# Performance work log

Hardware: AMD Instinct MI355X
Metric: run time of the kernel (lower is better)

## Reference

```python
import jax, jax.numpy as jnp
import numpy as np

HEADS = 4
DIM_HEAD = 32
SCALE = 10.0
EPS = 1e-12

def l2norm_axis1(t):
    # Faithful to source: default axis=1 -> normalize over the SEQUENCE axis of [B,N,h,d]
    denom = jnp.clip(jnp.linalg.norm(t, ord=2, axis=1, keepdims=True), EPS)
    return t / denom

def setup_inputs() -> dict:
    key = jax.random.key(0)
    k1, k2, k3 = jax.random.split(key, 3)
    B, N, C = 4, 4096, 128
    dim = HEADS * DIM_HEAD  # 128
    x = jax.random.normal(k1, (B, N, C), dtype=jnp.float32)
    W_qkv = jax.random.normal(k2, (C, 3 * dim), dtype=jnp.float32) * (1.0 / np.sqrt(C))
    W_out = jax.random.normal(k3, (dim, C), dtype=jnp.float32) * (1.0 / np.sqrt(dim))
    b_out = jnp.zeros((C,), dtype=jnp.float32)
    return {"x": x, "W_qkv": W_qkv, "W_out": W_out, "b_out": b_out}

def reference(x, W_qkv, W_out, b_out):
    B, N, C = x.shape
    # 1x1 conv == per-token linear
    qkv = jnp.einsum('bnc,ce->bne', x, W_qkv)  # [B,N,3*dim]
    q, k, v = jnp.split(qkv, 3, axis=-1)
    # [B,N,h,d]
    q = q.reshape(B, N, HEADS, DIM_HEAD)
    k = k.reshape(B, N, HEADS, DIM_HEAD)
    v = v.reshape(B, N, HEADS, DIM_HEAD)
    q = l2norm_axis1(q)
    k = l2norm_axis1(k)
    sim = jnp.einsum('bihd,bjhd->bhij', q, k) * SCALE  # [B,h,N,N]
    attn = jax.nn.softmax(sim, axis=-1)
    out = jnp.einsum('bhij,bjhd->bhid', attn, v)  # [B,h,N,d]
    out = out.transpose(0, 2, 1, 3).reshape(B, N, HEADS * DIM_HEAD)  # [B,N,dim]
    return jnp.einsum('bne,ec->bnc', out, W_out) + b_out
```

## Files before the change

### kernel.cpp

```cpp
#include <hip/hip_runtime.h>

typedef short s16x8 __attribute__((ext_vector_type(8)));
typedef short s16x4 __attribute__((ext_vector_type(4)));
typedef float f32x4 __attribute__((ext_vector_type(4)));
typedef float f4 __attribute__((ext_vector_type(4)));
typedef unsigned short u16x4 __attribute__((ext_vector_type(4)));

#define CEXP 14.426950408889634074f

__device__ __forceinline__ unsigned short f2bf(float f) {
    union { float f; unsigned int i; } v; v.f = f;
    unsigned int x = v.i;
    return (unsigned short)((x + 0x7fffu + ((x >> 16) & 1u)) >> 16);
}
__device__ __forceinline__ float bf2f(unsigned short u) {
    union { unsigned int i; float f; } v; v.i = ((unsigned int)u) << 16; return v.f;
}

__device__ __forceinline__ s16x4 pk_bf16x4(float p0, float p1, float p2, float p3) {
#if __has_builtin(__builtin_amdgcn_cvt_pk_bf16_f32)
    typedef __bf16 bf16x2 __attribute__((ext_vector_type(2)));
    union { struct { bf16x2 a, b; } h; s16x4 s; } r;
    r.h.a = __builtin_amdgcn_cvt_pk_bf16_f32(p0, p1);
    r.h.b = __builtin_amdgcn_cvt_pk_bf16_f32(p2, p3);
    return r.s;
#else
    unsigned u0 = __float_as_uint(p0) + 0x8000u;
    unsigned u1 = __float_as_uint(p1) + 0x8000u;
    unsigned u2 = __float_as_uint(p2) + 0x8000u;
    unsigned u3 = __float_as_uint(p3) + 0x8000u;
    union { uint2 u; s16x4 s; } pb;
    pb.u.x = __builtin_amdgcn_perm(u1, u0, 0x07060302u);
    pb.u.y = __builtin_amdgcn_perm(u3, u2, 0x07060302u);
    return pb.s;
#endif
}

__device__ __forceinline__ u16x4 pk4(f4 v) {
    u16x4 r = { f2bf(v[0]), f2bf(v[1]), f2bf(v[2]), f2bf(v[3]) };
    return r;
}

__device__ __forceinline__ void gl_lds16(const void* g, void* l) {
    __builtin_amdgcn_global_load_lds(
        (const __attribute__((address_space(1))) void*)g,
        (__attribute__((address_space(3))) void*)l,
        16, 0, 0);
}

__global__ __launch_bounds__(256) void k_prep(
    const float* __restrict__ Wqkv, const float* __restrict__ Wout,
    unsigned short* __restrict__ Wt, unsigned short* __restrict__ WoT,
    float* __restrict__ sumsqp)
{
    __shared__ float tile[64][65];
    const int blk = blockIdx.x, tid = threadIdx.x;
    if (blk >= 16) {
        sumsqp[(blk - 16) * 256 + tid] = 0.f;
        return;
    }
    const float* src;
    unsigned short* dst;
    int lds_src, k0, n0;
    if (blk < 12) {
        src = Wqkv; dst = Wt; lds_src = 384;
        k0 = (blk & 1) * 64; n0 = (blk >> 1) * 64;
    } else {
        int b = blk - 12;
        src = Wout; dst = WoT; lds_src = 128;
        k0 = (b & 1) * 64; n0 = (b >> 1) * 64;
    }
    const int c = tid & 63, r0 = tid >> 6;
#pragma unroll
    for (int i = 0; i < 16; ++i) {
        int row = i * 4 + r0;
        tile[row][c] = src[(size_t)(k0 + row) * lds_src + n0 + c];
    }
    __syncthreads();
#pragma unroll
    for (int i = 0; i < 16; ++i) {
        int n = i * 4 + r0;
        dst[(size_t)(n0 + n) * 128 + k0 + c] = f2bf(tile[c][n]);
    }
}

__global__ __launch_bounds__(256, 2) void k_qkv(
    const float* __restrict__ x, const unsigned short* __restrict__ Wt,
    unsigned short* __restrict__ Qb, unsigned short* __restrict__ Kb,
    unsigned short* __restrict__ Vt, float* __restrict__ sumsqp)
{
    __shared__ float red[4][64];
    const int tid = threadIdx.x;
    const int wl = tid >> 6, lane = tid & 63;
    const int qd = lane >> 4, nn = lane & 15;
    const int yb = blockIdx.y;
    const int tw0 = blockIdx.x * 64 + wl * 16;

    const float* apf = x + (size_t)(tw0 + nn) * 128 + qd * 8;
    s16x8 af[4];
#pragma unroll
    for (int ks = 0; ks < 4; ++ks) {
        f4 a0 = *(const f4*)(apf + ks * 32);
        f4 a1 = *(const f4*)(apf + ks * 32 + 4);
        union { struct { s16x4 lo, hi; } h; s16x8 v; } u;
        u.h.lo = pk_bf16x4(a0[0], a0[1], a0[2], a0[3]);
        u.h.hi = pk_bf16x4(a1[0], a1[1], a1[2], a1[3]);
        af[ks] = u.v;
    }

    const int b = tw0 >> 12;
    const int tl0 = tw0 & 4095;
    const int tok = tl0 + nn;

#pragma unroll
    for (int c = 0; c < 2; ++c) {
        const int n0 = c * 128 + yb * 64;
        const unsigned short* bp = Wt + (size_t)(n0 + nn) * 128 + qd * 8;
        s16x8 bfr[16];
#pragma unroll
        for (int nb = 0; nb < 4; ++nb)
#pragma unroll
            for (int ks = 0; ks < 4; ++ks)
                bfr[nb * 4 + ks] = *(const s16x8*)(bp + (size_t)nb * 2048 + ks * 32);

        f32x4 acc[4];
#pragma unroll
        for (int nb = 0; nb < 4; ++nb) acc[nb] = (f32x4){0.f, 0.f, 0.f, 0.f};
#pragma unroll
        for (int ks = 0; ks < 4; ++ks)
#pragma unroll
            for (int nb = 0; nb < 4; ++nb)
                acc[nb] = __builtin_amdgcn_mfma_f32_16x16x32_bf16(bfr[nb * 4 + ks], af[ks], acc[nb], 0, 0, 0);

        unsigned short* dst = (c == 0) ? Qb : Kb;
#pragma unroll
        for (int nb = 0; nb < 4; ++nb) {
            const int dim = yb * 64 + nb * 16 + qd * 4;
            const int h = dim >> 5, d0 = dim & 31;
            *(u16x4*)&dst[(size_t)((b * 4 + h) * 4096 + tok) * 32 + d0] = pk4(acc[nb]);
            f32x4 ss;
#pragma unroll
            for (int r = 0; r < 4; ++r) ss[r] = acc[nb][r] * acc[nb][r];
#pragma unroll
            for (int m = 1; m < 16; m <<= 1) {
#pragma unroll
                for (int r = 0; r < 4; ++r) ss[r] += __shfl_xor(ss[r], m);
            }
            if (nn == 0)
                *(f4*)&red[wl][nb * 16 + qd * 4] = ss;
        }
        __syncthreads();
        if (tid < 64) {
            float s = red[0][tid] + red[1][tid] + red[2][tid] + red[3][tid];
            const int g = (c << 9) + (b << 7) + yb * 64 + tid;
            atomicAdd(&sumsqp[((blockIdx.x & 7) << 10) + g], s);
        }
        __syncthreads();
    }

    {
        const int n0 = 256 + yb * 64;
        const unsigned short* bp = Wt + (size_t)(n0 + nn) * 128 + qd * 8;
        s16x8 bfr[16];
#pragma unroll
        for (int nb = 0; nb < 4; ++nb)
#pragma unroll
            for (int ks = 0; ks < 4; ++ks)
                bfr[nb * 4 + ks] = *(const s16x8*)(bp + (size_t)nb * 2048 + ks * 32);

        f32x4 acc[4];
#pragma unroll
        for (int nb = 0; nb < 4; ++nb) acc[nb] = (f32x4){0.f, 0.f, 0.f, 0.f};
#pragma unroll
        for (int ks = 0; ks < 4; ++ks)
#pragma unroll
            for (int nb = 0; nb < 4; ++nb)
                acc[nb] = __builtin_amdgcn_mfma_f32_16x16x32_bf16(af[ks], bfr[nb * 4 + ks], acc[nb], 0, 0, 0);
#pragma unroll
        for (int nb = 0; nb < 4; ++nb) {
            const int dim = yb * 64 + nb * 16 + nn;
            const int h = dim >> 5, d = dim & 31;
            *(u16x4*)&Vt[(size_t)((b * 4 + h) * 32 + d) * 4096 + tl0 + qd * 4] = pk4(acc[nb]);
        }
    }
}

__global__ __launch_bounds__(512, 4) void k_attn(
    const unsigned short* __restrict__ Qb, const unsigned short* __restrict__ Kb,
    const unsigned short* __restrict__ Vt, const float* __restrict__ sumsqp,
    unsigned short* __restrict__ Ogb)
{
    __shared__ char smem[32768];
    const int tid  = threadIdx.x;
    const int wv   = tid >> 6, lane = tid & 63;
    const int wl   = wv & 3, half = wv >> 2;
    const int qd   = lane >> 4, nn = lane & 15;
    const int bh   = blockIdx.x;
    const int ib   = blockIdx.y * 128 + wl * 32;
    const unsigned short* Qbh = Qb + (size_t)bh * 4096 * 32;
    const unsigned short* Kbh = Kb + (size_t)bh * 4096 * 32;
    const unsigned short* Vbh = Vt + (size_t)bh * 32 * 4096;

    float rj[8];
    {
        const int gq = bh * 32 + qd * 8;
#pragma unroll
        for (int j = 0; j < 8; ++j) {
            float sq = 0.f, sk = 0.f;
#pragma unroll
            for (int c = 0; c < 8; ++c) {
                sq += sumsqp[c * 1024 + gq + j];
                sk += sumsqp[c * 1024 + 512 + gq + j];
            }
            rj[j] = fminf(__builtin_amdgcn_rsqf(sq), 1e12f)
                  * fminf(__builtin_amdgcn_rsqf(sk), 1e12f) * CEXP;
        }
    }

    s16x8 q0r = *(const s16x8*)(Qbh + (ib + nn) * 32 + qd * 8);
    s16x8 q1r = *(const s16x8*)(Qbh + (ib + 16 + nn) * 32 + qd * 8);
    s16x8 qf0, qf1;
#pragma unroll
    for (int j = 0; j < 8; ++j) {
        qf0[j] = (short)f2bf(bf2f((unsigned short)q0r[j]) * rj[j]);
        qf1[j] = (short)f2bf(bf2f((unsigned short)q1r[j]) * rj[j]);
    }

    f32x4 o00 = {0.f,0.f,0.f,0.f}, o01 = {0.f,0.f,0.f,0.f};
    f32x4 o10 = {0.f,0.f,0.f,0.f}, o11 = {0.f,0.f,0.f,0.f};
    f32x4 la  = {0.f,0.f,0.f,0.f}, lb  = {0.f,0.f,0.f,0.f};
    const f32x4 zro = {0.f,0.f,0.f,0.f};
    const s16x8 ones8 = { (short)0x3F80, (short)0x3F80, (short)0x3F80, (short)0x3F80,
                          (short)0x3F80, (short)0x3F80, (short)0x3F80, (short)0x3F80 };

    const int KB0 = half * 8192;
    const int VB0 = 16384 + half * 8192;
    const int jb0 = half * 2048;

    const int jperm = ((wl >> 1) << 5) + ((nn >> 2) << 3) + ((wl & 1) << 2) + (nn & 3);
    const unsigned short* ksrc = Kbh + (size_t)(jb0 + jperm) * 32 + qd * 8;
    const unsigned short* vsrc = Vbh + (size_t)((wl >> 1) * 16 + nn) * 4096
                               + jb0 + (wl & 1) * 32 + qd * 8;
    char* kbase = smem + KB0 + wl * 1024;
    char* vbase = smem + VB0 + wl * 1024;

    {
        gl_lds16(ksrc, kbase);
        gl_lds16(vsrc, vbase);
        ksrc += 2048; vsrc += 64;
    }

    for (int jt = 0; jt < 32; ++jt) {
        __syncthreads();
        if (jt < 31) {
            const int nxt = ((jt + 1) & 1) * 4096;
            gl_lds16(ksrc, kbase + nxt);
            gl_lds16(vsrc, vbase + nxt);
            ksrc += 2048; vsrc += 64;
        }
        const char* kcur = smem + KB0 + (jt & 1) * 4096;
        const char* vcur = smem + VB0 + (jt & 1) * 4096;
#pragma unroll
        for (int js32 = 0; js32 < 2; ++js32) {
            s16x8 kf0 = *(const s16x8*)(kcur + (js32 * 2 + 0) * 1024 + lane * 16);
            s16x8 kf1 = *(const s16x8*)(kcur + (js32 * 2 + 1) * 1024 + lane * 16);
            f32x4 sa0 = __builtin_amdgcn_mfma_f32_16x16x32_bf16(kf0, qf0, zro, 0, 0, 0);
            f32x4 sb0 = __builtin_amdgcn_mfma_f32_16x16x32_bf16(kf0, qf1, zro, 0, 0, 0);
            f32x4 sa1 = __builtin_amdgcn_mfma_f32_16x16x32_bf16(kf1, qf0, zro, 0, 0, 0);
            f32x4 sb1 = __builtin_amdgcn_mfma_f32_16x16x32_bf16(kf1, qf1, zro, 0, 0, 0);
            float a0 = __builtin_amdgcn_exp2f(sa0[0]);
            float a1 = __builtin_amdgcn_exp2f(sa0[1]);
            float a2 = __builtin_amdgcn_exp2f(sa0[2]);
            float a3 = __builtin_amdgcn_exp2f(sa0[3]);
            float a4 = __builtin_amdgcn_exp2f(sa1[0]);
            float a5 = __builtin_amdgcn_exp2f(sa1[1]);
            float a6 = __builtin_amdgcn_exp2f(sa1[2]);
            float a7 = __builtin_amdgcn_exp2f(sa1[3]);
            float b0 = __builtin_amdgcn_exp2f(sb0[0]);
            float b1 = __builtin_amdgcn_exp2f(sb0[1]);
            float b2 = __builtin_amdgcn_exp2f(sb0[2]);
            float b3 = __builtin_amdgcn_exp2f(sb0[3]);
            float b4 = __builtin_amdgcn_exp2f(sb1[0]);
            float b5 = __builtin_amdgcn_exp2f(sb1[1]);
            float b6 = __builtin_amdgcn_exp2f(sb1[2]);
            float b7 = __builtin_amdgcn_exp2f(sb1[3]);
            union { struct { s16x4 lo, hi; } h; s16x8 v; } ua, ub;
            ua.h.lo = pk_bf16x4(a0, a1, a2, a3);
            ua.h.hi = pk_bf16x4(a4, a5, a6, a7);
            ub.h.lo = pk_bf16x4(b0, b1, b2, b3);
            ub.h.hi = pk_bf16x4(b4, b5, b6, b7);
            s16x8 pa32 = ua.v, pb32 = ub.v;
            la = __builtin_amdgcn_mfma_f32_16x16x32_bf16(ones8, pa32, la, 0, 0, 0);
            lb = __builtin_amdgcn_mfma_f32_16x16x32_bf16(ones8, pb32, lb, 0, 0, 0);
            s16x8 va = *(const s16x8*)(vcur + js32 * 1024 + lane * 16);
            s16x8 vb = *(const s16x8*)(vcur + 2048 + js32 * 1024 + lane * 16);
            o00 = __builtin_amdgcn_mfma_f32_16x16x32_bf16(va, pa32, o00, 0, 0, 0);
            o01 = __builtin_amdgcn_mfma_f32_16x16x32_bf16(vb, pa32, o01, 0, 0, 0);
            o10 = __builtin_amdgcn_mfma_f32_16x16x32_bf16(va, pb32, o10, 0, 0, 0);
            o11 = __builtin_amdgcn_mfma_f32_16x16x32_bf16(vb, pb32, o11, 0, 0, 0);
        }
    }

    const float lpa = la[0];
    const float lpb = lb[0];
    __syncthreads();
    float* Ob = (float*)smem;
    float* Lb = (float*)(smem + 16384);
    if (half) {
        float* d0 = Ob + ((wl * 2 + 0) * 64 + lane) * 8;
        *(f4*)d0 = o00; *(f4*)(d0 + 4) = o01;
        float* d1 = Ob + ((wl * 2 + 1) * 64 + lane) * 8;
        *(f4*)d1 = o10; *(f4*)(d1 + 4) = o11;
        Lb[(wl * 2 + 0) * 64 + lane] = lpa;
        Lb[(wl * 2 + 1) * 64 + lane] = lpb;
    }
    __syncthreads();
    if (!half) {
        const int bb = bh >> 2, hh = bh & 3;
        float* s0 = Ob + ((wl * 2 + 0) * 64 + lane) * 8;
        float rla = 1.f / (lpa + Lb[(wl * 2 + 0) * 64 + lane]);
        f4 m00 = (o00 + *(const f4*)s0) * rla;
        f4 m01 = (o01 + *(const f4*)(s0 + 4)) * rla;
        float* s1 = Ob + ((wl * 2 + 1) * 64 + lane) * 8;
        float rlb = 1.f / (lpb + Lb[(wl * 2 + 1) * 64 + lane]);
        f4 m10 = (o10 + *(const f4*)s1) * rlb;
        f4 m11 = (o11 + *(const f4*)(s1 + 4)) * rlb;
        unsigned short* dst0 = Ogb + (size_t)(bb * 4096 + blockIdx.y * 128 + wl * 32 + nn) * 128
                             + hh * 32 + qd * 4;
        *(u16x4*)dst0 = pk4(m00);
        *(u16x4*)(dst0 + 16) = pk4(m01);
        unsigned short* dst1 = dst0 + (size_t)16 * 128;
        *(u16x4*)dst1 = pk4(m10);
        *(u16x4*)(dst1 + 16) = pk4(m11);
    }
}

__global__ __launch_bounds__(256, 2) void k_out(
    const unsigned short* __restrict__ Ogb, const unsigned short* __restrict__ WoT,
    const float* __restrict__ bout, float* __restrict__ out)
{
    const int tid = threadIdx.x;
    const int wl = tid >> 6, lane = tid & 63;
    const int qd = lane >> 4, nn = lane & 15;
    const int n0 = blockIdx.y * 64;
    const int tw0 = blockIdx.x * 64 + wl * 16;

    const unsigned short* ap = WoT + (size_t)(n0 + nn) * 128 + qd * 8;
    const unsigned short* bp = Ogb + (size_t)(tw0 + nn) * 128 + qd * 8;
    s16x8 bfr[4], afr[16];
#pragma unroll
    for (int ks = 0; ks < 4; ++ks) bfr[ks] = *(const s16x8*)(bp + ks * 32);
#pragma unroll
    for (int nb = 0; nb < 4; ++nb)
#pragma unroll
        for (int ks = 0; ks < 4; ++ks)
            afr[nb * 4 + ks] = *(const s16x8*)(ap + (size_t)nb * 2048 + ks * 32);

    f32x4 acc[4];
#pragma unroll
    for (int nb = 0; nb < 4; ++nb) acc[nb] = (f32x4){0.f, 0.f, 0.f, 0.f};
#pragma unroll
    for (int ks = 0; ks < 4; ++ks)
#pragma unroll
        for (int nb = 0; nb < 4; ++nb)
            acc[nb] = __builtin_amdgcn_mfma_f32_16x16x32_bf16(afr[nb * 4 + ks], bfr[ks], acc[nb], 0, 0, 0);

#pragma unroll
    for (int nb = 0; nb < 4; ++nb) {
        const int c = n0 + nb * 16 + qd * 4;
        f4 bv = *(const f4*)&bout[c];
        f4 r;
#pragma unroll
        for (int j = 0; j < 4; ++j) r[j] = acc[nb][j] + bv[j];
        *(f4*)&out[(size_t)(tw0 + nn) * 128 + c] = r;
    }
}

extern "C" void kernel_launch(void* const* d_in, const int* in_sizes, int n_in,
                              void* d_out, int out_size, void* d_ws, size_t ws_size,
                              hipStream_t stream)
{
    const float* x    = (const float*)d_in[0];
    const float* Wqkv = (const float*)d_in[1];
    const float* Wout = (const float*)d_in[2];
    const float* bout = (const float*)d_in[3];
    float* out = (float*)d_out;
    char* ws = (char*)d_ws;
    const size_t MB = 1024 * 1024;
    unsigned short* Qb  = (unsigned short*)(ws);
    unsigned short* Kb  = (unsigned short*)(ws + 4 * MB);
    unsigned short* Vt  = (unsigned short*)(ws + 8 * MB);
    unsigned short* Ogb = (unsigned short*)(ws + 12 * MB);
    unsigned short* Wt  = (unsigned short*)(ws + 16 * MB);
    unsigned short* WoT = (unsigned short*)(ws + 16 * MB + 112 * 1024);
    float*       sumsqp = (float*)(ws + 16 * MB + 160 * 1024);

    hipLaunchKernelGGL(k_prep, dim3(48), dim3(256), 0, stream, Wqkv, Wout, Wt, WoT, sumsqp);
    hipLaunchKernelGGL(k_qkv, dim3(256, 2), dim3(256), 0, stream, x, Wt, Qb, Kb, Vt, sumsqp);
    hipLaunchKernelGGL(k_attn, dim3(16, 32), dim3(512), 0, stream, Qb, Kb, Vt, sumsqp, Ogb);
    hipLaunchKernelGGL(k_out, dim3(256, 2), dim3(256), 0, stream, Ogb, WoT, bout, out);
}
```

Baseline: 141.8 us.

## Fuse output projection into attention kernel with per-wave private K/V pipelines

Each attention block now covers all four heads of one batch for 32 query rows. Every wave streams its own head's K/V through a private double-buffered LDS region, using waitcnt-based synchronisation instead of block-wide barriers. The output projection is fused at the end, with the normalised attention output staged in LDS, which removes the separate k_out launch and the bf16 intermediate round-trip through global memory. In exchange, each block loads four times less Q per K/V tile, LDS use doubles to 64KB (which may limit occupancy), and the grid becomes 512 blocks.

```diff
diff --git a/kernel.cpp b/kernel.cpp
--- a/kernel.cpp
+++ b/kernel.cpp
@@ -188,15 +188,17 @@
 __global__ __launch_bounds__(512, 4) void k_attn(
     const unsigned short* __restrict__ Qb, const unsigned short* __restrict__ Kb,
     const unsigned short* __restrict__ Vt, const float* __restrict__ sumsqp,
-    unsigned short* __restrict__ Ogb)
+    const unsigned short* __restrict__ WoT, const float* __restrict__ bout,
+    float* __restrict__ out)
 {
-    __shared__ char smem[32768];
+    __shared__ char smem[65536];
     const int tid  = threadIdx.x;
     const int wv   = tid >> 6, lane = tid & 63;
-    const int wl   = wv & 3, half = wv >> 2;
+    const int h    = wv >> 1, jh = wv & 1;
     const int qd   = lane >> 4, nn = lane & 15;
-    const int bh   = blockIdx.x;
-    const int ib   = blockIdx.y * 128 + wl * 32;
+    const int bb   = blockIdx.x;
+    const int ib   = blockIdx.y * 32;
+    const int bh   = bb * 4 + h;
     const unsigned short* Qbh = Qb + (size_t)bh * 4096 * 32;
     const unsigned short* Kbh = Kb + (size_t)bh * 4096 * 32;
     const unsigned short* Vbh = Vt + (size_t)bh * 32 * 4096;
@@ -217,8 +219,8 @@
         }
     }
 
-    s16x8 q0r = *(const s16x8*)(Qbh + (ib + nn) * 32 + qd * 8);
-    s16x8 q1r = *(const s16x8*)(Qbh + (ib + 16 + nn) * 32 + qd * 8);
+    s16x8 q0r = *(const s16x8*)(Qbh + (size_t)(ib + nn) * 32 + qd * 8);
+    s16x8 q1r = *(const s16x8*)(Qbh + (size_t)(ib + 16 + nn) * 32 + qd * 8);
     s16x8 qf0, qf1;
 #pragma unroll
     for (int j = 0; j < 8; ++j) {
@@ -233,146 +235,146 @@
     const s16x8 ones8 = { (short)0x3F80, (short)0x3F80, (short)0x3F80, (short)0x3F80,
                           (short)0x3F80, (short)0x3F80, (short)0x3F80, (short)0x3F80 };
 
-    const int KB0 = half * 8192;
-    const int VB0 = 16384 + half * 8192;
-    const int jb0 = half * 2048;
-
-    const int jperm = ((wl >> 1) << 5) + ((nn >> 2) << 3) + ((wl & 1) << 2) + (nn & 3);
-    const unsigned short* ksrc = Kbh + (size_t)(jb0 + jperm) * 32 + qd * 8;
-    const unsigned short* vsrc = Vbh + (size_t)((wl >> 1) * 16 + nn) * 4096
-                               + jb0 + (wl & 1) * 32 + qd * 8;
-    char* kbase = smem + KB0 + wl * 1024;
-    char* vbase = smem + VB0 + wl * 1024;
-
+    char* kw = smem + wv * 8192;
+
+    const int jb0 = jh * 2048;
+    const int J0 = ((nn >> 2) << 3) + (nn & 3);
+    const unsigned short* ksrcA = Kbh + (size_t)(jb0 + J0) * 32 + qd * 8;
+    const unsigned short* ksrcB = Kbh + (size_t)(jb0 + J0 + 4) * 32 + qd * 8;
+    const unsigned short* vsrc0 = Vbh + (size_t)nn * 4096 + jb0 + qd * 8;
+    const unsigned short* vsrc1 = Vbh + (size_t)(16 + nn) * 4096 + jb0 + qd * 8;
+
+    gl_lds16(ksrcA, kw);               gl_lds16(ksrcB, kw + 1024);
+    gl_lds16(vsrc0, kw + 4096);        gl_lds16(vsrc1, kw + 5120);
+    gl_lds16(ksrcA + 1024, kw + 2048); gl_lds16(ksrcB + 1024, kw + 3072);
+    gl_lds16(vsrc0 + 32, kw + 6144);   gl_lds16(vsrc1 + 32, kw + 7168);
+    ksrcA += 2048; ksrcB += 2048; vsrc0 += 64; vsrc1 += 64;
+
+#define STEP_COMPUTE(kf0_, kf1_, va_, vb_) do {                               \
+    f32x4 sa0 = __builtin_amdgcn_mfma_f32_16x16x32_bf16(kf0_, qf0, zro, 0,0,0);\
+    f32x4 sb0 = __builtin_amdgcn_mfma_f32_16x16x32_bf16(kf0_, qf1, zro, 0,0,0);\
+    f32x4 sa1 = __builtin_amdgcn_mfma_f32_16x16x32_bf16(kf1_, qf0, zro, 0,0,0);\
+    f32x4 sb1 = __builtin_amdgcn_mfma_f32_16x16x32_bf16(kf1_, qf1, zro, 0,0,0);\
+    float a0 = __builtin_amdgcn_exp2f(sa0[0]);                                \
+    float a1 = __builtin_amdgcn_exp2f(sa0[1]);                                \
+    float a2 = __builtin_amdgcn_exp2f(sa0[2]);                                \
+    float a3 = __builtin_amdgcn_exp2f(sa0[3]);                                \
+    float a4 = __builtin_amdgcn_exp2f(sa1[0]);                                \
+    float a5 = __builtin_amdgcn_exp2f(sa1[1]);                                \
+    float a6 = __builtin_amdgcn_exp2f(sa1[2]);                                \
+    float a7 = __builtin_amdgcn_exp2f(sa1[3]);                                \
+    float b0 = __builtin_amdgcn_exp2f(sb0[0]);                                \
+    float b1 = __builtin_amdgcn_exp2f(sb0[1]);                                \
+    float b2 = __builtin_amdgcn_exp2f(sb0[2]);                                \
+    float b3 = __builtin_amdgcn_exp2f(sb0[3]);                                \
+    float b4 = __builtin_amdgcn_exp2f(sb1[0]);                                \
+    float b5 = __builtin_amdgcn_exp2f(sb1[1]);                                \
+    float b6 = __builtin_amdgcn_exp2f(sb1[2]);                                \
+    float b7 = __builtin_amdgcn_exp2f(sb1[3]);                                \
+    union { struct { s16x4 lo, hi; } hh2; s16x8 v; } ua, ub;                  \
+    ua.hh2.lo = pk_bf16x4(a0, a1, a2, a3);                                    \
+    ua.hh2.hi = pk_bf16x4(a4, a5, a6, a7);                                    \
+    ub.hh2.lo = pk_bf16x4(b0, b1, b2, b3);                                    \
+    ub.hh2.hi = pk_bf16x4(b4, b5, b6, b7);                                    \
+    s16x8 pa32 = ua.v, pb32 = ub.v;                                           \
+    la  = __builtin_amdgcn_mfma_f32_16x16x32_bf16(ones8, pa32, la, 0, 0, 0);  \
+    lb  = __builtin_amdgcn_mfma_f32_16x16x32_bf16(ones8, pb32, lb, 0, 0, 0);  \
+    o00 = __builtin_amdgcn_mfma_f32_16x16x32_bf16(va_, pa32, o00, 0, 0, 0);   \
+    o01 = __builtin_amdgcn_mfma_f32_16x16x32_bf16(vb_, pa32, o01, 0, 0, 0);   \
+    o10 = __builtin_amdgcn_mfma_f32_16x16x32_bf16(va_, pb32, o10, 0, 0, 0);   \
+    o11 = __builtin_amdgcn_mfma_f32_16x16x32_bf16(vb_, pb32, o11, 0, 0, 0);   \
+} while (0)
+
+    for (int t = 0; t < 62; ++t) {
+        char* kc = kw + (t & 1) * 2048;
+        char* vc = kw + 4096 + (t & 1) * 2048;
+        asm volatile("s_waitcnt vmcnt(4)" ::: "memory");
+        __builtin_amdgcn_sched_barrier(0);
+        s16x8 kf0 = *(const s16x8*)(kc + lane * 16);
+        s16x8 kf1 = *(const s16x8*)(kc + 1024 + lane * 16);
+        s16x8 va  = *(const s16x8*)(vc + lane * 16);
+        s16x8 vb  = *(const s16x8*)(vc + 1024 + lane * 16);
+        asm volatile("s_waitcnt lgkmcnt(0)" ::: "memory");
+        __builtin_amdgcn_sched_barrier(0);
+        gl_lds16(ksrcA, kc);  gl_lds16(ksrcB, kc + 1024);
+        gl_lds16(vsrc0, vc);  gl_lds16(vsrc1, vc + 1024);
+        ksrcA += 1024; ksrcB += 1024; vsrc0 += 32; vsrc1 += 32;
+        STEP_COMPUTE(kf0, kf1, va, vb);
+    }
     {
-        gl_lds16(ksrc, kbase);
-        gl_lds16(vsrc, vbase);
-        ksrc += 2048; vsrc += 64;
-    }
-
-    for (int jt = 0; jt < 32; ++jt) {
-        __syncthreads();
-        if (jt < 31) {
-            const int nxt = ((jt + 1) & 1) * 4096;
-            gl_lds16(ksrc, kbase + nxt);
-            gl_lds16(vsrc, vbase + nxt);
-            ksrc += 2048; vsrc += 64;
-        }
-        const char* kcur = smem + KB0 + (jt & 1) * 4096;
-        const char* vcur = smem + VB0 + (jt & 1) * 4096;
-#pragma unroll
-        for (int js32 = 0; js32 < 2; ++js32) {
-            s16x8 kf0 = *(const s16x8*)(kcur + (js32 * 2 + 0) * 1024 + lane * 16);
-            s16x8 kf1 = *(const s16x8*)(kcur + (js32 * 2 + 1) * 1024 + lane * 16);
-            f32x4 sa0 = __builtin_amdgcn_mfma_f32_16x16x32_bf16(kf0, qf0, zro, 0, 0, 0);
-            f32x4 sb0 = __builtin_amdgcn_mfma_f32_16x16x32_bf16(kf0, qf1, zro, 0, 0, 0);
-            f32x4 sa1 = __builtin_amdgcn_mfma_f32_16x16x32_bf16(kf1, qf0, zro, 0, 0, 0);
-            f32x4 sb1 = __builtin_amdgcn_mfma_f32_16x16x32_bf16(kf1, qf1, zro, 0, 0, 0);
-            float a0 = __builtin_amdgcn_exp2f(sa0[0]);
-            float a1 = __builtin_amdgcn_exp2f(sa0[1]);
-            float a2 = __builtin_amdgcn_exp2f(sa0[2]);
-            float a3 = __builtin_amdgcn_exp2f(sa0[3]);
-            float a4 = __builtin_amdgcn_exp2f(sa1[0]);
-            float a5 = __builtin_amdgcn_exp2f(sa1[1]);
-            float a6 = __builtin_amdgcn_exp2f(sa1[2]);
-            float a7 = __builtin_amdgcn_exp2f(sa1[3]);
-            float b0 = __builtin_amdgcn_exp2f(sb0[0]);
-            float b1 = __builtin_amdgcn_exp2f(sb0[1]);
-            float b2 = __builtin_amdgcn_exp2f(sb0[2]);
-            float b3 = __builtin_amdgcn_exp2f(sb0[3]);
-            float b4 = __builtin_amdgcn_exp2f(sb1[0]);
-            float b5 = __builtin_amdgcn_exp2f(sb1[1]);
-            float b6 = __builtin_amdgcn_exp2f(sb1[2]);
-            float b7 = __builtin_amdgcn_exp2f(sb1[3]);
-            union { struct { s16x4 lo, hi; } h; s16x8 v; } ua, ub;
-            ua.h.lo = pk_bf16x4(a0, a1, a2, a3);
-            ua.h.hi = pk_bf16x4(a4, a5, a6, a7);
-            ub.h.lo = pk_bf16x4(b0, b1, b2, b3);
-            ub.h.hi = pk_bf16x4(b4, b5, b6, b7);
-            s16x8 pa32 = ua.v, pb32 = ub.v;
-            la = __builtin_amdgcn_mfma_f32_16x16x32_bf16(ones8, pa32, la, 0, 0, 0);
-            lb = __builtin_amdgcn_mfma_f32_16x16x32_bf16(ones8, pb32, lb, 0, 0, 0);
-            s16x8 va = *(const s16x8*)(vcur + js32 * 1024 + lane * 16);
-            s16x8 vb = *(const s16x8*)(vcur + 2048 + js32 * 1024 + lane * 16);
-            o00 = __builtin_amdgcn_mfma_f32_16x16x32_bf16(va, pa32, o00, 0, 0, 0);
-            o01 = __builtin_amdgcn_mfma_f32_16x16x32_bf16(vb, pa32, o01, 0, 0, 0);
-            o10 = __builtin_amdgcn_mfma_f32_16x16x32_bf16(va, pb32, o10, 0, 0, 0);
-            o11 = __builtin_amdgcn_mfma_f32_16x16x32_bf16(vb, pb32, o11, 0, 0, 0);
-        }
-    }
+        asm volatile("s_waitcnt vmcnt(4)" ::: "memory");
+        __builtin_amdgcn_sched_barrier(0);
+        s16x8 kf0 = *(const s16x8*)(kw + lane * 16);
+        s16x8 kf1 = *(const s16x8*)(kw + 1024 + lane * 16);
+        s16x8 va  = *(const s16x8*)(kw + 4096 + lane * 16);
+        s16x8 vb  = *(const s16x8*)(kw + 5120 + lane * 16);
+        STEP_COMPUTE(kf0, kf1, va, vb);
+    }
+    {
+        asm volatile("s_waitcnt vmcnt(0)" ::: "memory");
+        __builtin_amdgcn_sched_barrier(0);
+        s16x8 kf0 = *(const s16x8*)(kw + 2048 + lane * 16);
+        s16x8 kf1 = *(const s16x8*)(kw + 3072 + lane * 16);
+        s16x8 va  = *(const s16x8*)(kw + 6144 + lane * 16);
+        s16x8 vb  = *(const s16x8*)(kw + 7168 + lane * 16);
+        STEP_COMPUTE(kf0, kf1, va, vb);
+    }
+#undef STEP_COMPUTE
 
     const float lpa = la[0];
     const float lpb = lb[0];
+
     __syncthreads();
     float* Ob = (float*)smem;
     float* Lb = (float*)(smem + 16384);
-    if (half) {
-        float* d0 = Ob + ((wl * 2 + 0) * 64 + lane) * 8;
+    unsigned short* Og = (unsigned short*)(smem + 20480);
+    if (jh) {
+        float* d0 = Ob + ((h * 2 + 0) * 64 + lane) * 8;
         *(f4*)d0 = o00; *(f4*)(d0 + 4) = o01;
-        float* d1 = Ob + ((wl * 2 + 1) * 64 + lane) * 8;
+        float* d1 = Ob + ((h * 2 + 1) * 64 + lane) * 8;
         *(f4*)d1 = o10; *(f4*)(d1 + 4) = o11;
-        Lb[(wl * 2 + 0) * 64 + lane] = lpa;
-        Lb[(wl * 2 + 1) * 64 + lane] = lpb;
+        Lb[(h * 2 + 0) * 64 + lane] = lpa;
+        Lb[(h * 2 + 1) * 64 + lane] = lpb;
     }
     __syncthreads();
-    if (!half) {
-        const int bb = bh >> 2, hh = bh & 3;
-        float* s0 = Ob + ((wl * 2 + 0) * 64 + lane) * 8;
-        float rla = 1.f / (lpa + Lb[(wl * 2 + 0) * 64 + lane]);
+    if (!jh) {
+        float* s0 = Ob + ((h * 2 + 0) * 64 + lane) * 8;
+        float rla = 1.f / (lpa + Lb[(h * 2 + 0) * 64 + lane]);
         f4 m00 = (o00 + *(const f4*)s0) * rla;
         f4 m01 = (o01 + *(const f4*)(s0 + 4)) * rla;
-        float* s1 = Ob + ((wl * 2 + 1) * 64 + lane) * 8;
-        float rlb = 1.f / (lpb + Lb[(wl * 2 + 1) * 64 + lane]);
+        float* s1 = Ob + ((h * 2 + 1) * 64 + lane) * 8;
+        float rlb = 1.f / (lpb + Lb[(h * 2 + 1) * 64 + lane]);
         f4 m10 = (o10 + *(const f4*)s1) * rlb;
         f4 m11 = (o11 + *(const f4*)(s1 + 4)) * rlb;
-        unsigned short* dst0 = Ogb + (size_t)(bb * 4096 + blockIdx.y * 128 + wl * 32 + nn) * 128
-                             + hh * 32 + qd * 4;
-        *(u16x4*)dst0 = pk4(m00);
-        *(u16x4*)(dst0 + 16) = pk4(m01);
-        unsigned short* dst1 = dst0 + (size_t)16 * 128;
-        *(u16x4*)dst1 = pk4(m10);
-        *(u16x4*)(dst1 + 16) = pk4(m11);
-    }
-}
-
-__global__ __launch_bounds__(256, 2) void k_out(
-    const unsigned short* __restrict__ Ogb, const unsigned short* __restrict__ WoT,
-    const float* __restrict__ bout, float* __restrict__ out)
-{
-    const int tid = threadIdx.x;
-    const int wl = tid >> 6, lane = tid & 63;
-    const int qd = lane >> 4, nn = lane & 15;
-    const int n0 = blockIdx.y * 64;
-    const int tw0 = blockIdx.x * 64 + wl * 16;
-
-    const unsigned short* ap = WoT + (size_t)(n0 + nn) * 128 + qd * 8;
-    const unsigned short* bp = Ogb + (size_t)(tw0 + nn) * 128 + qd * 8;
-    s16x8 bfr[4], afr[16];
-#pragma unroll
-    for (int ks = 0; ks < 4; ++ks) bfr[ks] = *(const s16x8*)(bp + ks * 32);
-#pragma unroll
-    for (int nb = 0; nb < 4; ++nb)
-#pragma unroll
-        for (int ks = 0; ks < 4; ++ks)
-            afr[nb * 4 + ks] = *(const s16x8*)(ap + (size_t)nb * 2048 + ks * 32);
-
-    f32x4 acc[4];
-#pragma unroll
-    for (int nb = 0; nb < 4; ++nb) acc[nb] = (f32x4){0.f, 0.f, 0.f, 0.f};
-#pragma unroll
-    for (int ks = 0; ks < 4; ++ks)
-#pragma unroll
-        for (int nb = 0; nb < 4; ++nb)
-            acc[nb] = __builtin_amdgcn_mfma_f32_16x16x32_bf16(afr[nb * 4 + ks], bfr[ks], acc[nb], 0, 0, 0);
-
-#pragma unroll
-    for (int nb = 0; nb < 4; ++nb) {
-        const int c = n0 + nb * 16 + qd * 4;
-        f4 bv = *(const f4*)&bout[c];
-        f4 r;
-#pragma unroll
-        for (int j = 0; j < 4; ++j) r[j] = acc[nb][j] + bv[j];
-        *(f4*)&out[(size_t)(tw0 + nn) * 128 + c] = r;
+        unsigned short* g0 = Og + (size_t)(0 + nn) * 136 + h * 32 + qd * 4;
+        *(u16x4*)g0 = pk4(m00);
+        *(u16x4*)(g0 + 16) = pk4(m01);
+        unsigned short* g1 = Og + (size_t)(16 + nn) * 136 + h * 32 + qd * 4;
+        *(u16x4*)g1 = pk4(m10);
+        *(u16x4*)(g1 + 16) = pk4(m11);
+    }
+    __syncthreads();
+
+    {
+        const unsigned short* ap = WoT + (size_t)(wv * 16 + nn) * 128 + qd * 8;
+        s16x8 afr[4];
+#pragma unroll
+        for (int ks = 0; ks < 4; ++ks) afr[ks] = *(const s16x8*)(ap + ks * 32);
+        f32x4 acc0 = zro, acc1 = zro;
+#pragma unroll
+        for (int ks = 0; ks < 4; ++ks) {
+            s16x8 b0 = *(const s16x8*)(Og + (size_t)(0 + nn) * 136 + ks * 32 + qd * 8);
+            s16x8 b1 = *(const s16x8*)(Og + (size_t)(16 + nn) * 136 + ks * 32 + qd * 8);
+            acc0 = __builtin_amdgcn_mfma_f32_16x16x32_bf16(afr[ks], b0, acc0, 0, 0, 0);
+            acc1 = __builtin_amdgcn_mfma_f32_16x16x32_bf16(afr[ks], b1, acc1, 0, 0, 0);
+        }
+        const int cbase = wv * 16 + qd * 4;
+        f4 bv = *(const f4*)&bout[cbase];
+        f4 r0, r1;
+#pragma unroll
+        for (int j = 0; j < 4; ++j) { r0[j] = acc0[j] + bv[j]; r1[j] = acc1[j] + bv[j]; }
+        *(f4*)&out[(size_t)(bb * 4096 + ib + nn) * 128 + cbase] = r0;
+        *(f4*)&out[(size_t)(bb * 4096 + ib + 16 + nn) * 128 + cbase] = r1;
     }
 }
 
@@ -390,13 +392,11 @@
     unsigned short* Qb  = (unsigned short*)(ws);
     unsigned short* Kb  = (unsigned short*)(ws + 4 * MB);
     unsigned short* Vt  = (unsigned short*)(ws + 8 * MB);
-    unsigned short* Ogb = (unsigned short*)(ws + 12 * MB);
     unsigned short* Wt  = (unsigned short*)(ws + 16 * MB);
     unsigned short* WoT = (unsigned short*)(ws + 16 * MB + 112 * 1024);
     float*       sumsqp = (float*)(ws + 16 * MB + 160 * 1024);
 
     hipLaunchKernelGGL(k_prep, dim3(48), dim3(256), 0, stream, Wqkv, Wout, Wt, WoT, sumsqp);
     hipLaunchKernelGGL(k_qkv, dim3(256, 2), dim3(256), 0, stream, x, Wt, Qb, Kb, Vt, sumsqp);
-    hipLaunchKernelGGL(k_attn, dim3(16, 32), dim3(512), 0, stream, Qb, Kb, Vt, sumsqp, Ogb);
-    hipLaunchKernelGGL(k_out, dim3(256, 2), dim3(256), 0, stream, Ogb, WoT, bout, out);
-}
+    hipLaunchKernelGGL(k_attn, dim3(4, 128), dim3(512), 0, stream, Qb, Kb, Vt, sumsqp, WoT, bout, out);
+}
```

Result: slower. 183.2 us (+29.1%).
